# Optimization experiments

Measured on AMD Instinct MI355X. Metric: run time of the kernel, lower is better.

## Reference

```python
import jax, jax.numpy as jnp
import numpy as np

B, N, C, H = 1, 4096, 512, 8
S = 64  # sqrt(N), static


def setup_inputs() -> dict:
    key = jax.random.key(0)
    ks = jax.random.split(key, 4)
    d = C // H
    return {
        "x": jax.random.normal(ks[0], (B, N, C), dtype=jnp.float32),
        "num_heads": H,
        "bias": jnp.zeros((1,), dtype=jnp.float32),  # unused in original forward
        "scale": jnp.asarray(d ** -0.5, dtype=jnp.float32),
        "Wqkv": jax.random.normal(ks[1], (3 * C, C), dtype=jnp.float32) * (C ** -0.5),
        "bqkv": jnp.zeros((3 * C,), dtype=jnp.float32),
        "Wproj": jax.random.normal(ks[2], (C, C), dtype=jnp.float32) * (C ** -0.5),
        "bproj": jnp.zeros((C,), dtype=jnp.float32),
    }


def reference(x, num_heads, bias, scale, Wqkv, bqkv, Wproj, bproj):
    b, n, c = x.shape
    d = c // num_heads
    # fused QKV projection: [b, n, 3c] -> [3, b, h, n, d]
    qkv = (x @ Wqkv.T + bqkv).reshape(b, n, 3, num_heads, d).transpose(2, 0, 3, 1, 4)
    q, k, v = qkv[0] * scale, qkv[1], qkv[2]
    attn = jax.nn.softmax(jnp.einsum("bhnd,bhmd->bhnm", q, k), axis=-1)
    out = jnp.einsum("bhnm,bhmd->bhnd", attn, v)
    out = out.transpose(0, 2, 1, 3).reshape(b, n, c)
    out = out @ Wproj.T + bproj
    return out.reshape(b, S, S, c)
```

## Files before the change

### kernel.cpp

```cpp
#include <hip/hip_runtime.h>
#include <stdint.h>

#define NTOK 4096
#define CDIM 512
#define HEADS 8
#define DHEAD 64
#define PHEAD (NTOK * DHEAD)
#define LDS_K 40

typedef __bf16 bf16x8 __attribute__((ext_vector_type(8)));
typedef float f32x4 __attribute__((ext_vector_type(4)));

__device__ __forceinline__ unsigned short bfbits(float f) {
    return __builtin_bit_cast(unsigned short, (__bf16)f);
}

__device__ __forceinline__ f32x4 mfma32(bf16x8 a, bf16x8 b, f32x4 c) {
    return __builtin_amdgcn_mfma_f32_16x16x32_bf16(a, b, c, 0, 0, 0);
}

__device__ __forceinline__ void cvt_store8(unsigned short* dst, float4 v0, float4 v1) {
    ushort4 o0, o1;
    o0.x = bfbits(v0.x); o0.y = bfbits(v0.y); o0.z = bfbits(v0.z); o0.w = bfbits(v0.w);
    o1.x = bfbits(v1.x); o1.y = bfbits(v1.y); o1.z = bfbits(v1.z); o1.w = bfbits(v1.w);
    *(ushort4*)dst = o0;
    *(ushort4*)(dst + 4) = o1;
}

__global__ __launch_bounds__(256) void gemm_qkv(
    const float* __restrict__ A,
    const float* __restrict__ Bm,
    const float* __restrict__ bias,
    const float* __restrict__ scale_p,
    unsigned short* __restrict__ qkv_out)
{
    __shared__ __align__(16) unsigned short smem[64 * 136];
    unsigned short* lA = smem;
    unsigned short* lB = smem + 64 * LDS_K;

    const int tid = threadIdx.x;
    const int mBase = blockIdx.y * 64, nBase = blockIdx.x * 128;
    const int lane = tid & 63;
    const int w = __builtin_amdgcn_readfirstlane(tid >> 6);
    const int l16 = lane & 15, quad = lane >> 4;
    const int srow = tid >> 2, scol = (tid & 3) * 8;

    const float* pA  = &A[(size_t)(mBase + srow) * CDIM + scol];
    const float* pB0 = &Bm[(size_t)(nBase + srow) * CDIM + scol];
    const float* pB1 = &Bm[(size_t)(nBase + 64 + srow) * CDIM + scol];

    f32x4 acc[4][2] = {};

    float4 ra0, ra1, rb00, rb01, rb10, rb11;
    auto issue = [&](int kt) {
        ra0  = *(const float4*)(pA + kt);
        ra1  = *(const float4*)(pA + kt + 4);
        rb00 = *(const float4*)(pB0 + kt);
        rb01 = *(const float4*)(pB0 + kt + 4);
        rb10 = *(const float4*)(pB1 + kt);
        rb11 = *(const float4*)(pB1 + kt + 4);
    };
    issue(0);

    for (int kt = 0; kt < CDIM; kt += 32) {
        __syncthreads();
        cvt_store8(&lA[srow * LDS_K + scol], ra0, ra1);
        cvt_store8(&lB[srow * LDS_K + scol], rb00, rb01);
        cvt_store8(&lB[(64 + srow) * LDS_K + scol], rb10, rb11);
        __syncthreads();
        if (kt + 32 < CDIM) issue(kt + 32);

        bf16x8 af[4], bfr[2];
#pragma unroll
        for (int i = 0; i < 4; ++i)
            af[i] = *(const bf16x8*)&lA[(i * 16 + l16) * LDS_K + quad * 8];
#pragma unroll
        for (int j = 0; j < 2; ++j)
            bfr[j] = *(const bf16x8*)&lB[(w * 32 + j * 16 + l16) * LDS_K + quad * 8];
#pragma unroll
        for (int i = 0; i < 4; ++i)
#pragma unroll
            for (int j = 0; j < 2; ++j)
                acc[i][j] = mfma32(af[i], bfr[j], acc[i][j]);
    }

    const int three = nBase >> 9;
    const float scl = scale_p[0] * 1.44269504f;
    const float mul = (three == 0) ? scl : 1.0f;

    __syncthreads();
#pragma unroll
    for (int i = 0; i < 4; ++i)
#pragma unroll
        for (int j = 0; j < 2; ++j)
#pragma unroll
            for (int r = 0; r < 4; ++r) {
                const int rl = i * 16 + quad * 4 + r;
                const int cl = w * 32 + j * 16 + l16;
                const float v = (acc[i][j][r] + bias[nBase + cl]) * mul;
                smem[rl * 136 + cl] = bfbits(v);
            }
    __syncthreads();

    const size_t base3 = (size_t)three * (PHEAD * HEADS);
    if (three < 2) {
#pragma unroll
        for (int pass = 0; pass < 4; ++pass) {
            const int idx = pass * 256 + tid;
            const int rl16 = idx & 15, qc = (idx >> 4) & 7;
            const int hsel = (idx >> 7) & 1, t16l = (idx >> 8) & 3;
            const uint4 d = *(const uint4*)&smem[(t16l * 16 + rl16) * 136 + hsel * 64 + qc * 8];
            const int hh = ((nBase >> 6) + hsel) & 7;
            const int t16 = (mBase >> 4) + t16l;
            const size_t dst = base3 + (size_t)hh * PHEAD +
                (size_t)(((t16 * 2 + (qc >> 2)) * 64 + (qc & 3) * 16 + rl16) * 8);
            *(uint4*)&qkv_out[dst] = d;
        }
    } else {
#pragma unroll
        for (int pass = 0; pass < 4; ++pass) {
            const int idx = pass * 256 + tid;
            const int l16t = idx & 15, quadt = (idx >> 4) & 3;
            const int dt = (idx >> 6) & 3, k32l = (idx >> 8) & 1, hsel = (idx >> 9) & 1;
            const int col = hsel * 64 + dt * 16 + l16t;
            unsigned short o8[8];
#pragma unroll
            for (int e = 0; e < 4; ++e) {
                o8[e]     = smem[(k32l * 32 + quadt * 4 + e) * 136 + col];
                o8[e + 4] = smem[(k32l * 32 + 16 + quadt * 4 + e) * 136 + col];
            }
            const int hh = ((nBase >> 6) + hsel) & 7;
            const int k32 = (mBase >> 5) + k32l;
            const size_t dst = base3 + (size_t)hh * PHEAD +
                (size_t)(((k32 * 4 + dt) * 64 + quadt * 16 + l16t) * 8);
            *(uint4*)&qkv_out[dst] = *(uint4*)o8;
        }
    }
}

__global__ __launch_bounds__(256, 2) void flash7_k(
    const unsigned short* __restrict__ qf,
    const unsigned short* __restrict__ kf,
    const unsigned short* __restrict__ vf,
    unsigned short* __restrict__ attn_out)
{
    __shared__ float ldsO[4][64][68];
    __shared__ float sml[4][64];

    const int tid = threadIdx.x;
    const int lane = tid & 63;
    const int w = __builtin_amdgcn_readfirstlane(tid >> 6);
    const int l16 = lane & 15, quad = lane >> 4;
    const int h = blockIdx.x, qb = blockIdx.y;

    const unsigned short* qh = qf + (size_t)h * PHEAD;
    const unsigned short* kb = kf + (size_t)h * PHEAD + w * 65536;
    const unsigned short* vb = vf + (size_t)h * PHEAD + w * 65536;

    bf16x8 qfr[4][2];
#pragma unroll
    for (int qt = 0; qt < 4; ++qt)
#pragma unroll
        for (int d2 = 0; d2 < 2; ++d2)
            qfr[qt][d2] = *(const bf16x8*)&qh[((qb * 4 + qt) * 2 + d2) * 512 + lane * 8];

    bf16x8 ones;
#pragma unroll
    for (int j = 0; j < 8; ++j) ones[j] = (__bf16)1.0f;

    f32x4 oacc[4][4] = {};
    f32x4 lacc[4] = {};

    bf16x8 kA[4], kB[4];
#pragma unroll
    for (int i = 0; i < 4; ++i)
        kA[i] = *(const bf16x8*)&kb[i * 512 + lane * 8];

    auto body = [&](int g, bf16x8* kuse, bf16x8* kload) {
#pragma unroll
        for (int i = 0; i < 4; ++i)
            kload[i] = *(const bf16x8*)&kb[(g + 1) * 2048 + i * 512 + lane * 8];
        bf16x8 vc[4];
#pragma unroll
        for (int i = 0; i < 4; ++i)
            vc[i] = *(const bf16x8*)&vb[g * 2048 + i * 512 + lane * 8];

        bf16x8 pf[4];
#pragma unroll
        for (int qt = 0; qt < 4; ++qt) {
            f32x4 s0 = {}, s1 = {};
            s0 = mfma32(kuse[0], qfr[qt][0], s0);
            s0 = mfma32(kuse[1], qfr[qt][1], s0);
            s1 = mfma32(kuse[2], qfr[qt][0], s1);
            s1 = mfma32(kuse[3], qfr[qt][1], s1);
            bf16x8 pb;
#pragma unroll
            for (int r = 0; r < 4; ++r) {
                pb[r]     = (__bf16)__builtin_amdgcn_exp2f(s0[r]);
                pb[4 + r] = (__bf16)__builtin_amdgcn_exp2f(s1[r]);
            }
            pf[qt] = pb;
            lacc[qt] = mfma32(ones, pb, lacc[qt]);
        }
#pragma unroll
        for (int dt = 0; dt < 4; ++dt)
#pragma unroll
            for (int qt = 0; qt < 4; ++qt)
                oacc[dt][qt] = mfma32(vc[dt], pf[qt], oacc[dt][qt]);
    };

    for (int it = 0; it < 16; ++it) {
        body(it * 2 + 0, kA, kB);
        body(it * 2 + 1, kB, kA);
    }

    if (quad == 0) {
#pragma unroll
        for (int qt = 0; qt < 4; ++qt) sml[w][qt * 16 + l16] = lacc[qt][0];
    }
#pragma unroll
    for (int qt = 0; qt < 4; ++qt) {
        const int q = qt * 16 + l16;
#pragma unroll
        for (int dt = 0; dt < 4; ++dt)
            *(f32x4*)&ldsO[w][q][dt * 16 + quad * 4] = oacc[dt][qt];
    }
    __syncthreads();
#pragma unroll
    for (int pass = 0; pass < 2; ++pass) {
        const int idx = pass * 256 + tid;
        const int q = idx >> 3, dseg = (idx & 7) * 8;
        const float L = sml[0][q] + sml[1][q] + sml[2][q] + sml[3][q];
        const float inv = 1.f / L;
        unsigned short o8[8];
#pragma unroll
        for (int i = 0; i < 8; ++i) {
            const float v = ldsO[0][q][dseg + i] + ldsO[1][q][dseg + i] +
                            ldsO[2][q][dseg + i] + ldsO[3][q][dseg + i];
            o8[i] = bfbits(v * inv);
        }
        *(uint4*)&attn_out[(size_t)(qb * 64 + q) * CDIM + h * DHEAD + dseg] = *(uint4*)o8;
    }
}

__global__ __launch_bounds__(256) void gemm_proj(
    const unsigned short* __restrict__ A,
    const float* __restrict__ Bm,
    const float* __restrict__ bias,
    float* __restrict__ c_out)
{
    __shared__ __align__(16) unsigned short smem[2 * 64 * LDS_K];
    unsigned short* lA = smem;
    unsigned short* lB = smem + 64 * LDS_K;

    const int tid = threadIdx.x;
    const int mBase = blockIdx.y * 64, nBase = blockIdx.x * 64;
    const int lane = tid & 63;
    const int w = __builtin_amdgcn_readfirstlane(tid >> 6);
    const int l16 = lane & 15, quad = lane >> 4;
    const int srow = tid >> 2, scol = (tid & 3) * 8;

    const unsigned short* pA = &A[(size_t)(mBase + srow) * CDIM + scol];
    const float* pB = &Bm[(size_t)(nBase + srow) * CDIM + scol];

    f32x4 acc[4] = {};

    uint4 rA; float4 rb0, rb1;
    auto issue = [&](int kt) {
        rA  = *(const uint4*)(pA + kt);
        rb0 = *(const float4*)(pB + kt);
        rb1 = *(const float4*)(pB + kt + 4);
    };
    issue(0);

    for (int kt = 0; kt < CDIM; kt += 32) {
        __syncthreads();
        *(uint4*)&lA[srow * LDS_K + scol] = rA;
        cvt_store8(&lB[srow * LDS_K + scol], rb0, rb1);
        __syncthreads();
        if (kt + 32 < CDIM) issue(kt + 32);

        bf16x8 af[4], bfr;
#pragma unroll
        for (int i = 0; i < 4; ++i)
            af[i] = *(const bf16x8*)&lA[(i * 16 + l16) * LDS_K + quad * 8];
        bfr = *(const bf16x8*)&lB[(w * 16 + l16) * LDS_K + quad * 8];
#pragma unroll
        for (int i = 0; i < 4; ++i)
            acc[i] = mfma32(af[i], bfr, acc[i]);
    }

#pragma unroll
    for (int i = 0; i < 4; ++i)
#pragma unroll
        for (int r = 0; r < 4; ++r) {
            const int grow = mBase + i * 16 + quad * 4 + r;
            const int gcol = nBase + w * 16 + l16;
            c_out[(size_t)grow * CDIM + gcol] = acc[i][r] + bias[gcol];
        }
}

extern "C" void kernel_launch(void* const* d_in, const int* in_sizes, int n_in,
                              void* d_out, int out_size, void* d_ws, size_t ws_size,
                              hipStream_t stream) {
    const float* x       = (const float*)d_in[0];
    const float* scale_p = (const float*)d_in[3];
    const float* Wqkv    = (const float*)d_in[4];
    const float* bqkv    = (const float*)d_in[5];
    const float* Wproj   = (const float*)d_in[6];
    const float* bproj   = (const float*)d_in[7];
    float* out = (float*)d_out;

    char* ws = (char*)d_ws;
    const size_t OFF_QKV  = 0;
    const size_t OFF_ATTN = 12582912;
    const size_t NEEDED   = OFF_ATTN + 4194304;
    if (ws_size < NEEDED) return;

    unsigned short* qkvb  = (unsigned short*)(ws + OFF_QKV);
    unsigned short* attnb = (unsigned short*)(ws + OFF_ATTN);

    gemm_qkv<<<dim3(12, 64), 256, 0, stream>>>(x, Wqkv, bqkv, scale_p, qkvb);

    const unsigned short* qfr = qkvb;
    const unsigned short* kfr = qkvb + (size_t)PHEAD * HEADS;
    const unsigned short* vfr = qkvb + (size_t)2 * PHEAD * HEADS;
    flash7_k<<<dim3(8, 64), 256, 0, stream>>>(qfr, kfr, vfr, attnb);

    gemm_proj<<<dim3(8, 64), 256, 0, stream>>>(attnb, Wproj, bproj, out);
}
```

Before: 136.1 us.

## Double K-step in GEMMs, prefetch V and compute row sums on VALU in attention

Both projection GEMMs now stage 64-wide K slices per barrier pair instead of 32, with a wider LDS stride, which halves synchronisation and load-issue overhead. The attention kernel double-buffers V alongside K, computes the softmax denominator with VALU adds and cross-lane shuffles instead of an MFMA against a ones vector, and raises wave priority around the MFMA blocks. These aim to cut barrier stalls, memory latency exposure and matrix-core work, at the cost of more registers and VALU instructions.

```diff
diff --git a/kernel.cpp b/kernel.cpp
--- a/kernel.cpp
+++ b/kernel.cpp
@@ -6,7 +6,7 @@
 #define HEADS 8
 #define DHEAD 64
 #define PHEAD (NTOK * DHEAD)
-#define LDS_K 40
+#define LDS_K 72
 
 typedef __bf16 bf16x8 __attribute__((ext_vector_type(8)));
 typedef float f32x4 __attribute__((ext_vector_type(4)));
@@ -34,7 +34,7 @@
     const float* __restrict__ scale_p,
     unsigned short* __restrict__ qkv_out)
 {
-    __shared__ __align__(16) unsigned short smem[64 * 136];
+    __shared__ __align__(16) unsigned short smem[64 * LDS_K + 128 * LDS_K];
     unsigned short* lA = smem;
     unsigned short* lB = smem + 64 * LDS_K;
 
@@ -43,45 +43,49 @@
     const int lane = tid & 63;
     const int w = __builtin_amdgcn_readfirstlane(tid >> 6);
     const int l16 = lane & 15, quad = lane >> 4;
-    const int srow = tid >> 2, scol = (tid & 3) * 8;
-
-    const float* pA  = &A[(size_t)(mBase + srow) * CDIM + scol];
-    const float* pB0 = &Bm[(size_t)(nBase + srow) * CDIM + scol];
-    const float* pB1 = &Bm[(size_t)(nBase + 64 + srow) * CDIM + scol];
+
+    const int rA = tid >> 2, cA = (tid & 3) * 16;
+    const int rB = tid >> 1, cB = (tid & 1) * 32;
+    const float* pA = &A[(size_t)(mBase + rA) * CDIM + cA];
+    const float* pB = &Bm[(size_t)(nBase + rB) * CDIM + cB];
 
     f32x4 acc[4][2] = {};
 
-    float4 ra0, ra1, rb00, rb01, rb10, rb11;
+    float4 ra[4], rb[8];
     auto issue = [&](int kt) {
-        ra0  = *(const float4*)(pA + kt);
-        ra1  = *(const float4*)(pA + kt + 4);
-        rb00 = *(const float4*)(pB0 + kt);
-        rb01 = *(const float4*)(pB0 + kt + 4);
-        rb10 = *(const float4*)(pB1 + kt);
-        rb11 = *(const float4*)(pB1 + kt + 4);
+#pragma unroll
+        for (int u = 0; u < 4; ++u) ra[u] = *(const float4*)(pA + kt + u * 4);
+#pragma unroll
+        for (int u = 0; u < 8; ++u) rb[u] = *(const float4*)(pB + kt + u * 4);
     };
     issue(0);
 
-    for (int kt = 0; kt < CDIM; kt += 32) {
+    for (int kt = 0; kt < CDIM; kt += 64) {
         __syncthreads();
-        cvt_store8(&lA[srow * LDS_K + scol], ra0, ra1);
-        cvt_store8(&lB[srow * LDS_K + scol], rb00, rb01);
-        cvt_store8(&lB[(64 + srow) * LDS_K + scol], rb10, rb11);
+        cvt_store8(&lA[rA * LDS_K + cA], ra[0], ra[1]);
+        cvt_store8(&lA[rA * LDS_K + cA + 8], ra[2], ra[3]);
+        cvt_store8(&lB[rB * LDS_K + cB], rb[0], rb[1]);
+        cvt_store8(&lB[rB * LDS_K + cB + 8], rb[2], rb[3]);
+        cvt_store8(&lB[rB * LDS_K + cB + 16], rb[4], rb[5]);
+        cvt_store8(&lB[rB * LDS_K + cB + 24], rb[6], rb[7]);
         __syncthreads();
-        if (kt + 32 < CDIM) issue(kt + 32);
-
-        bf16x8 af[4], bfr[2];
-#pragma unroll
-        for (int i = 0; i < 4; ++i)
-            af[i] = *(const bf16x8*)&lA[(i * 16 + l16) * LDS_K + quad * 8];
-#pragma unroll
-        for (int j = 0; j < 2; ++j)
-            bfr[j] = *(const bf16x8*)&lB[(w * 32 + j * 16 + l16) * LDS_K + quad * 8];
-#pragma unroll
-        for (int i = 0; i < 4; ++i)
+        if (kt + 64 < CDIM) issue(kt + 64);
+
+#pragma unroll
+        for (int kk = 0; kk < 64; kk += 32) {
+            bf16x8 af[4], bfr[2];
+#pragma unroll
+            for (int i = 0; i < 4; ++i)
+                af[i] = *(const bf16x8*)&lA[(i * 16 + l16) * LDS_K + kk + quad * 8];
 #pragma unroll
             for (int j = 0; j < 2; ++j)
-                acc[i][j] = mfma32(af[i], bfr[j], acc[i][j]);
+                bfr[j] = *(const bf16x8*)&lB[(w * 32 + j * 16 + l16) * LDS_K + kk + quad * 8];
+#pragma unroll
+            for (int i = 0; i < 4; ++i)
+#pragma unroll
+                for (int j = 0; j < 2; ++j)
+                    acc[i][j] = mfma32(af[i], bfr[j], acc[i][j]);
+        }
     }
 
     const int three = nBase >> 9;
@@ -138,7 +142,7 @@
     }
 }
 
-__global__ __launch_bounds__(256, 2) void flash7_k(
+__global__ __launch_bounds__(256, 2) void flash8_k(
     const unsigned short* __restrict__ qf,
     const unsigned short* __restrict__ kf,
     const unsigned short* __restrict__ vf,
@@ -164,59 +168,80 @@
         for (int d2 = 0; d2 < 2; ++d2)
             qfr[qt][d2] = *(const bf16x8*)&qh[((qb * 4 + qt) * 2 + d2) * 512 + lane * 8];
 
-    bf16x8 ones;
-#pragma unroll
-    for (int j = 0; j < 8; ++j) ones[j] = (__bf16)1.0f;
-
     f32x4 oacc[4][4] = {};
-    f32x4 lacc[4] = {};
-
-    bf16x8 kA[4], kB[4];
-#pragma unroll
-    for (int i = 0; i < 4; ++i)
+    float lv[4] = {};
+
+    bf16x8 kA[4], kB[4], vA[4], vB[4];
+#pragma unroll
+    for (int i = 0; i < 4; ++i) {
         kA[i] = *(const bf16x8*)&kb[i * 512 + lane * 8];
-
-    auto body = [&](int g, bf16x8* kuse, bf16x8* kload) {
+        vA[i] = *(const bf16x8*)&vb[i * 512 + lane * 8];
+    }
+
+    auto body = [&](int g, bf16x8* kuse, bf16x8* kload, bf16x8* vuse, bf16x8* vload) {
+        const int gn = (g + 1) & 31;
 #pragma unroll
         for (int i = 0; i < 4; ++i)
-            kload[i] = *(const bf16x8*)&kb[(g + 1) * 2048 + i * 512 + lane * 8];
-        bf16x8 vc[4];
+            kload[i] = *(const bf16x8*)&kb[gn * 2048 + i * 512 + lane * 8];
 #pragma unroll
         for (int i = 0; i < 4; ++i)
-            vc[i] = *(const bf16x8*)&vb[g * 2048 + i * 512 + lane * 8];
+            vload[i] = *(const bf16x8*)&vb[gn * 2048 + i * 512 + lane * 8];
+
+        f32x4 s0[4], s1[4];
+        __builtin_amdgcn_s_setprio(1);
+#pragma unroll
+        for (int qt = 0; qt < 4; ++qt) {
+            f32x4 a = {};
+            a = mfma32(kuse[0], qfr[qt][0], a);
+            a = mfma32(kuse[1], qfr[qt][1], a);
+            s0[qt] = a;
+            f32x4 b = {};
+            b = mfma32(kuse[2], qfr[qt][0], b);
+            b = mfma32(kuse[3], qfr[qt][1], b);
+            s1[qt] = b;
+        }
+        __builtin_amdgcn_s_setprio(0);
 
         bf16x8 pf[4];
 #pragma unroll
         for (int qt = 0; qt < 4; ++qt) {
-            f32x4 s0 = {}, s1 = {};
-            s0 = mfma32(kuse[0], qfr[qt][0], s0);
-            s0 = mfma32(kuse[1], qfr[qt][1], s0);
-            s1 = mfma32(kuse[2], qfr[qt][0], s1);
-            s1 = mfma32(kuse[3], qfr[qt][1], s1);
+            float e0[4], e1[4];
+#pragma unroll
+            for (int r = 0; r < 4; ++r) {
+                e0[r] = __builtin_amdgcn_exp2f(s0[qt][r]);
+                e1[r] = __builtin_amdgcn_exp2f(s1[qt][r]);
+            }
+            lv[qt] += ((e0[0] + e0[1]) + (e0[2] + e0[3])) +
+                      ((e1[0] + e1[1]) + (e1[2] + e1[3]));
             bf16x8 pb;
 #pragma unroll
             for (int r = 0; r < 4; ++r) {
-                pb[r]     = (__bf16)__builtin_amdgcn_exp2f(s0[r]);
-                pb[4 + r] = (__bf16)__builtin_amdgcn_exp2f(s1[r]);
+                pb[r]     = (__bf16)e0[r];
+                pb[4 + r] = (__bf16)e1[r];
             }
             pf[qt] = pb;
-            lacc[qt] = mfma32(ones, pb, lacc[qt]);
-        }
+        }
+
+        __builtin_amdgcn_s_setprio(1);
 #pragma unroll
         for (int dt = 0; dt < 4; ++dt)
 #pragma unroll
             for (int qt = 0; qt < 4; ++qt)
-                oacc[dt][qt] = mfma32(vc[dt], pf[qt], oacc[dt][qt]);
+                oacc[dt][qt] = mfma32(vuse[dt], pf[qt], oacc[dt][qt]);
+        __builtin_amdgcn_s_setprio(0);
     };
 
     for (int it = 0; it < 16; ++it) {
-        body(it * 2 + 0, kA, kB);
-        body(it * 2 + 1, kB, kA);
-    }
-
-    if (quad == 0) {
-#pragma unroll
-        for (int qt = 0; qt < 4; ++qt) sml[w][qt * 16 + l16] = lacc[qt][0];
+        body(it * 2 + 0, kA, kB, vA, vB);
+        body(it * 2 + 1, kB, kA, vB, vA);
+    }
+
+#pragma unroll
+    for (int qt = 0; qt < 4; ++qt) {
+        float L = lv[qt];
+        L += __shfl_xor(L, 16, 64);
+        L += __shfl_xor(L, 32, 64);
+        if (quad == 0) sml[w][qt * 16 + l16] = L;
     }
 #pragma unroll
     for (int qt = 0; qt < 4; ++qt) {
@@ -258,36 +283,42 @@
     const int lane = tid & 63;
     const int w = __builtin_amdgcn_readfirstlane(tid >> 6);
     const int l16 = lane & 15, quad = lane >> 4;
-    const int srow = tid >> 2, scol = (tid & 3) * 8;
-
-    const unsigned short* pA = &A[(size_t)(mBase + srow) * CDIM + scol];
-    const float* pB = &Bm[(size_t)(nBase + srow) * CDIM + scol];
+
+    const int rT = tid >> 2, cT = (tid & 3) * 16;
+    const unsigned short* pA = &A[(size_t)(mBase + rT) * CDIM + cT];
+    const float* pB = &Bm[(size_t)(nBase + rT) * CDIM + cT];
 
     f32x4 acc[4] = {};
 
-    uint4 rA; float4 rb0, rb1;
+    uint4 rA0, rA1; float4 rb[4];
     auto issue = [&](int kt) {
-        rA  = *(const uint4*)(pA + kt);
-        rb0 = *(const float4*)(pB + kt);
-        rb1 = *(const float4*)(pB + kt + 4);
+        rA0 = *(const uint4*)(pA + kt);
+        rA1 = *(const uint4*)(pA + kt + 8);
+#pragma unroll
+        for (int u = 0; u < 4; ++u) rb[u] = *(const float4*)(pB + kt + u * 4);
     };
     issue(0);
 
-    for (int kt = 0; kt < CDIM; kt += 32) {
+    for (int kt = 0; kt < CDIM; kt += 64) {
         __syncthreads();
-        *(uint4*)&lA[srow * LDS_K + scol] = rA;
-        cvt_store8(&lB[srow * LDS_K + scol], rb0, rb1);
+        *(uint4*)&lA[rT * LDS_K + cT]     = rA0;
+        *(uint4*)&lA[rT * LDS_K + cT + 8] = rA1;
+        cvt_store8(&lB[rT * LDS_K + cT], rb[0], rb[1]);
+        cvt_store8(&lB[rT * LDS_K + cT + 8], rb[2], rb[3]);
         __syncthreads();
-        if (kt + 32 < CDIM) issue(kt + 32);
-
-        bf16x8 af[4], bfr;
-#pragma unroll
-        for (int i = 0; i < 4; ++i)
-            af[i] = *(const bf16x8*)&lA[(i * 16 + l16) * LDS_K + quad * 8];
-        bfr = *(const bf16x8*)&lB[(w * 16 + l16) * LDS_K + quad * 8];
-#pragma unroll
-        for (int i = 0; i < 4; ++i)
-            acc[i] = mfma32(af[i], bfr, acc[i]);
+        if (kt + 64 < CDIM) issue(kt + 64);
+
+#pragma unroll
+        for (int kk = 0; kk < 64; kk += 32) {
+            bf16x8 af[4], bfr;
+#pragma unroll
+            for (int i = 0; i < 4; ++i)
+                af[i] = *(const bf16x8*)&lA[(i * 16 + l16) * LDS_K + kk + quad * 8];
+            bfr = *(const bf16x8*)&lB[(w * 16 + l16) * LDS_K + kk + quad * 8];
+#pragma unroll
+            for (int i = 0; i < 4; ++i)
+                acc[i] = mfma32(af[i], bfr, acc[i]);
+        }
     }
 
 #pragma unroll
@@ -325,7 +356,7 @@
     const unsigned short* qfr = qkvb;
     const unsigned short* kfr = qkvb + (size_t)PHEAD * HEADS;
     const unsigned short* vfr = qkvb + (size_t)2 * PHEAD * HEADS;
-    flash7_k<<<dim3(8, 64), 256, 0, stream>>>(qfr, kfr, vfr, attnb);
+    flash8_k<<<dim3(8, 64), 256, 0, stream>>>(qfr, kfr, vfr, attnb);
 
     gemm_proj<<<dim3(8, 64), 256, 0, stream>>>(attnb, Wproj, bproj, out);
 }
```

New measurement: 146.4 us. 7.6% more time.
